# Performance work log

Hardware: AMD Instinct MI355X
Metric: run time of the kernel (lower is better)

## Reference

```python
import jax, jax.numpy as jnp
import numpy as np

B, OBS, ACT, NT, E, H1, H2, D = 4096, 390, 20, 10, 8, 1024, 512, 256


def setup_inputs() -> dict:
    key = jax.random.key(0)
    ks = jax.random.split(key, 16)
    f32 = jnp.float32

    def w(k, shape, fan_in):
        return jax.random.normal(k, shape, f32) / np.float32(np.sqrt(fan_in))

    return {
        "state_feat": jax.random.normal(ks[0], (B, OBS), f32),
        "act": jax.random.normal(ks[1], (B, ACT), f32),
        "task_id": jax.random.randint(ks[2], (B,), 0, NT, jnp.int32),
        "rep_W1": w(ks[3], (OBS + ACT, H1), OBS + ACT),
        "rep_b1": jnp.zeros((H1,), f32),
        "rep_W2": w(ks[4], (H1, H1), H1),
        "rep_b2": jnp.zeros((H1,), f32),
        "emb": 0.5 * jax.random.normal(ks[5], (NT, D), f32),
        "kW1": w(ks[6], (E, H1, H2), H1),
        "kb1": jnp.zeros((E, H2), f32),
        "kW2": w(ks[7], (E, H2, D), H2),
        "kb2": jnp.zeros((E, D), f32),
        "vW1": w(ks[8], (E, H1, H2), H1),
        "vb1": jnp.zeros((E, H2), f32),
        "vW2": w(ks[9], (E, H2, D), H2),
        "vb2": jnp.zeros((E, D), f32),
        "tW1": w(ks[10], (D, D), D),
        "tb1": jnp.zeros((D,), f32),
        "tW2": w(ks[11], (D, D), D),
        "tb2": jnp.zeros((D,), f32),
        "tW3": w(ks[12], (D, 1), D),
        "tb3": jnp.zeros((1,), f32),
    }


def reference(state_feat, act, task_id, rep_W1, rep_b1, rep_W2, rep_b2, emb,
              kW1, kb1, kW2, kb2, vW1, vb1, vW2, vb2,
              tW1, tb1, tW2, tb2, tW3, tb3):
    # representation: mlp([obs+act, 1024, 1024]) -> ReLU on first layer only
    x = jnp.concatenate([state_feat, act], axis=-1)              # [B, 410]
    rep = jnp.maximum(x @ rep_W1 + rep_b1, 0.0) @ rep_W2 + rep_b2  # [B, H1]
    query = jnp.tanh(emb[task_id])                               # [B, D]

    # batched per-expert key/value MLPs (grouped GEMM instead of python loop)
    hk = jnp.maximum(jnp.einsum('bi,eio->ebo', rep, kW1) + kb1[:, None, :], 0.0)
    keys = jnp.einsum('ebo,eod->ebd', hk, kW2) + kb2[:, None, :]   # [E, B, D]
    hv = jnp.maximum(jnp.einsum('bi,eio->ebo', rep, vW1) + vb1[:, None, :], 0.0)
    vals = jnp.einsum('ebo,eod->ebd', hv, vW2) + vb2[:, None, :]   # [E, B, D]

    scores = jnp.einsum('bd,ebd->be', query, keys)               # [B, E]
    weight = jax.nn.softmax(scores, axis=1)                      # [B, E]
    tower_in = jnp.einsum('be,ebd->bd', weight, vals)            # [B, D]

    # tower: mlp([256, 256, 256, 1]) -> ReLU, ReLU, Identity
    h = jnp.maximum(tower_in @ tW1 + tb1, 0.0)
    h = jnp.maximum(h @ tW2 + tb2, 0.0)
    q = (h @ tW3 + tb3)[:, 0]                                    # [B]

    expert_loss = -jnp.mean(
        jnp.sum(jnp.clip(jnp.log(weight + 1e-10), -6.0, 0.0), axis=-1) * 0.3)
    return q, expert_loss
```

## Files before the change

### kernel.cpp

```cpp
#include <hip/hip_runtime.h>

constexpr int Bn   = 4096;
constexpr int OBS  = 390;
constexpr int ACTN = 20;
constexpr int IN   = 410;
constexpr int KPAD = 416;
constexpr int E    = 8;
constexpr int H1   = 1024;
constexpr int H2   = 512;
constexpr int D    = 256;

typedef __bf16 bf16x8 __attribute__((ext_vector_type(8)));
typedef float  f32x4  __attribute__((ext_vector_type(4)));

__device__ __forceinline__ unsigned short f2bf(float f) {
    unsigned int u = __float_as_uint(f);
    unsigned int r = u + 0x7fffu + ((u >> 16) & 1u);
    return (unsigned short)(r >> 16);
}
__device__ __forceinline__ void gload16(void* lds_dst, const void* g_src) {
    __builtin_amdgcn_global_load_lds(
        (const __attribute__((address_space(1))) void*)g_src,
        (__attribute__((address_space(3))) void*)lds_dst,
        16, 0, 0);
}

__global__ void prep_kernel(const float* __restrict__ sf, const float* __restrict__ ac,
                            unsigned short* __restrict__ x,
                            const float* __restrict__ emb, const int* __restrict__ task_id,
                            float* __restrict__ query) {
    int idx = blockIdx.x * blockDim.x + threadIdx.x;
    if (idx < Bn * KPAD) {
        int b = idx / KPAD;
        int k = idx - b * KPAD;
        float v = 0.f;
        if (k < OBS) v = sf[b * OBS + k];
        else if (k < IN) v = ac[b * ACTN + (k - OBS)];
        x[idx] = f2bf(v);
    } else {
        int j = idx - Bn * KPAD;
        int b = j >> 8;
        int d = j & 255;
        query[j] = tanhf(emb[task_id[b] * D + d]);
    }
}

struct TDesc {
    const float* W;
    unsigned short* WT;
    int K, N, Kpad;
    long long gsW, gsO;
    int tilesX, tilesY, perG;
    int start;
};
struct TDescArr { TDesc d[8]; };

__global__ __launch_bounds__(256) void mega_transpose(TDescArr da) {
    int bid = blockIdx.x;
    int i = 0;
#pragma unroll
    for (int j = 1; j < 8; ++j) if (bid >= da.d[j].start) i = j;
    TDesc dd = da.d[i];
    int local = bid - dd.start;
    int g   = local / dd.perG;
    int rem = local - g * dd.perG;
    int tyt = rem / dd.tilesX;
    int txt = rem - tyt * dd.tilesX;
    const float* W = dd.W + (long long)g * dd.gsW;
    unsigned short* WT = dd.WT + (long long)g * dd.gsO;

    __shared__ float tile[32][33];
    int tx = threadIdx.x & 31, ty = threadIdx.x >> 5;
    int k0 = tyt * 32, n0 = txt * 32;
#pragma unroll
    for (int r = 0; r < 4; ++r) {
        int k = k0 + ty + r * 8;
        tile[ty + r * 8][tx] = (k < dd.K) ? W[(long long)k * dd.N + n0 + tx] : 0.f;
    }
    __syncthreads();
#pragma unroll
    for (int r = 0; r < 4; ++r) {
        int n = n0 + ty + r * 8;
        WT[(long long)n * dd.Kpad + k0 + tx] = f2bf(tile[tx][ty + r * 8]);
    }
}

__global__ void bias_concat(const float* __restrict__ kb1, const float* __restrict__ vb1,
                            const float* __restrict__ kb2, const float* __restrict__ vb2,
                            float* __restrict__ b1cat, float* __restrict__ b2cat) {
    int i = blockIdx.x * blockDim.x + threadIdx.x;
    if (i < E * H2)            b1cat[i] = kb1[i];
    else if (i < 2 * E * H2)   b1cat[i] = vb1[i - E * H2];
    else {
        int j = i - 2 * E * H2;
        if (j < E * D)         b2cat[j] = kb2[j];
        else                   b2cat[j] = vb2[j - E * D];
    }
}

template <int ACTF, int OUTF, int BK>
__global__ __launch_bounds__(256) void gemm_bf16(
    const unsigned short* __restrict__ A, const unsigned short* __restrict__ BT,
    const float* __restrict__ bias, void* __restrict__ Cout,
    int K, int ldc,
    long long gsA, long long gsBT, long long gsBias, long long gsC)
{
    constexpr int CH   = BK / 8;
    constexpr int RPR  = 256 / CH;
    constexpr int RNDS = 128 / RPR;
    constexpr int TB   = 128 * BK * 2;
    constexpr int RS   = CH * 16;

    const int g = blockIdx.z;
    A    += (long long)g * gsA;
    BT   += (long long)g * gsBT;
    bias += (long long)g * gsBias;
    float*          Cf = (float*)Cout + (long long)g * gsC;
    unsigned short* Cb = (unsigned short*)Cout + (long long)g * gsC;

    __shared__ alignas(16) char smem[2 * TB];
    const int t  = threadIdx.x;
    const int w  = t >> 6, l = t & 63;
    const int lr = l & 15, lk = l >> 4;
    const int gm = blockIdx.y * 128, gn = blockIdx.x * 128;
    const int wm = (w >> 1) * 64,   wn = (w & 1) * 64;

    const int srow = t / CH;
    const int swzS = (CH == 8) ? (srow & 7) : ((srow >> 1) & 3);
    const int sc   = (t % CH) ^ swzS;
    const unsigned short* gA = A  + (long long)(gm + srow) * K + sc * 8;
    const unsigned short* gB = BT + (long long)(gn + srow) * K + sc * 8;

    const int swzL = (CH == 8) ? (lr & 7) : ((lr >> 1) & 3);
    const int aoff = (wm + lr) * RS + ((lk ^ swzL) * 16);
    const int boff = TB + (wn + lr) * RS + ((lk ^ swzL) * 16);

    f32x4 acc[4][4] = {};

    for (int k0 = 0; k0 < K; k0 += BK) {
#pragma unroll
        for (int j = 0; j < RNDS; ++j) {
            gload16(smem + j * 4096 + w * 1024,      gA + k0 + (long long)j * RPR * K);
            gload16(smem + TB + j * 4096 + w * 1024, gB + k0 + (long long)j * RPR * K);
        }
        __syncthreads();

        bf16x8 af[4], bfr[4];
#pragma unroll
        for (int i = 0; i < 4; ++i) {
            af[i]  = *(const bf16x8*)(smem + aoff + i * 16 * RS);
            bfr[i] = *(const bf16x8*)(smem + boff + i * 16 * RS);
        }
#pragma unroll
        for (int mi = 0; mi < 4; ++mi)
#pragma unroll
            for (int ni = 0; ni < 4; ++ni)
                acc[mi][ni] = __builtin_amdgcn_mfma_f32_16x16x32_bf16(
                    af[mi], bfr[ni], acc[mi][ni], 0, 0, 0);

        if constexpr (BK == 64) {
#pragma unroll
            for (int i = 0; i < 4; ++i) {
                af[i]  = *(const bf16x8*)(smem + (aoff ^ 64) + i * 16 * RS);
                bfr[i] = *(const bf16x8*)(smem + (boff ^ 64) + i * 16 * RS);
            }
#pragma unroll
            for (int mi = 0; mi < 4; ++mi)
#pragma unroll
                for (int ni = 0; ni < 4; ++ni)
                    acc[mi][ni] = __builtin_amdgcn_mfma_f32_16x16x32_bf16(
                        af[mi], bfr[ni], acc[mi][ni], 0, 0, 0);
        }
        __syncthreads();
    }

    const int orow0 = gm + wm + lk * 4;
    const int ocol0 = gn + wn + lr;
    float bv[4];
#pragma unroll
    for (int ni = 0; ni < 4; ++ni) bv[ni] = bias[gn + wn + lr + ni * 16];
#pragma unroll
    for (int mi = 0; mi < 4; ++mi)
#pragma unroll
        for (int ni = 0; ni < 4; ++ni)
#pragma unroll
            for (int r = 0; r < 4; ++r) {
                float v = acc[mi][ni][r] + bv[ni];
                if (ACTF == 1) v = fmaxf(v, 0.f);
                long long off = (long long)(orow0 + mi * 16 + r) * ldc + ocol0 + ni * 16;
                if (OUTF == 0) Cf[off] = v;
                else           Cb[off] = f2bf(v);
            }
}

template <int KTOT, int ACTF, int OUTF>
__global__ __launch_bounds__(512, 2) void gemm256(
    const unsigned short* __restrict__ A, const unsigned short* __restrict__ BT,
    const float* __restrict__ bias, void* __restrict__ Cout,
    int ldc, long long gsA, long long gsBT, long long gsBias, long long gsC)
{
    constexpr int NT = KTOT / 64;
    static_assert(NT >= 4 && (NT % 2) == 0, "KTOT must be multiple of 128");

    const int g = blockIdx.z;
    A    += (long long)g * gsA;
    BT   += (long long)g * gsBT;
    bias += (long long)g * gsBias;
    float*          Cf = (float*)Cout + (long long)g * gsC;
    unsigned short* Cb = (unsigned short*)Cout + (long long)g * gsC;

    __shared__ __align__(16) char smem[131072];

    const int tid = threadIdx.x;
    const int l  = tid & 63;
    const int lr = l & 15, lk = l >> 4;
    const int w  = tid >> 6;
    const int wr = w >> 2, wc = w & 3;
    const int gm = blockIdx.y * 256, gn = blockIdx.x * 256;

    const int srow = tid >> 3;
    const int cg   = (tid & 7) ^ (srow & 7);
    const unsigned short* gA = A  + (long long)(gm + srow) * KTOT + cg * 8;
    const unsigned short* gB = BT + (long long)(gn + srow) * KTOT + cg * 8;
    const int wbase = (tid & ~63) * 16;

    const int cs0 = ((0 | lk) ^ (lr & 7)) * 16;
    const int cs1 = ((4 | lk) ^ (lr & 7)) * 16;
    const int aRow = wr * 16384 + lr * 128;
    const int bRow = 32768 + (wc >> 1) * 16384 + ((wc & 1) * 64 + lr) * 128;

    f32x4 acc[8][4] = {};

    auto stA = [&](int c, int s, int kt) {
        const unsigned short* src = gA + (long long)(s * 128) * KTOT + kt * 64;
        char* d = smem + c * 65536 + s * 16384 + wbase;
        gload16(d,        src);
        gload16(d + 8192, src + (long long)64 * KTOT);
    };
    auto stB = [&](int c, int s, int kt) {
        const unsigned short* src = gB + (long long)(s * 128) * KTOT + kt * 64;
        char* d = smem + c * 65536 + 32768 + s * 16384 + wbase;
        gload16(d,        src);
        gload16(d + 8192, src + (long long)64 * KTOT);
    };

    stA(0, 0, 0); stA(0, 1, 0); stB(0, 0, 0); stB(0, 1, 0);
    stA(1, 0, 1); stA(1, 1, 1);
    asm volatile("s_waitcnt vmcnt(4)" ::: "memory");
    __builtin_amdgcn_s_barrier();
    __builtin_amdgcn_sched_barrier(0);

#pragma unroll
    for (int kt = 0; kt < NT; ++kt) {
        const int c = kt & 1;
        const char* bufc = smem + c * 65536;
        bf16x8 a0[4], a1[4], b0[4], b1[4];

#pragma unroll
        for (int m = 0; m < 4; ++m) {
            const char* base = bufc + aRow + m * (16 * 128);
            a0[m] = *(const bf16x8*)(base + cs0);
            a1[m] = *(const bf16x8*)(base + cs1);
        }
#pragma unroll
        for (int n = 0; n < 4; ++n) {
            const char* base = bufc + bRow + n * (16 * 128);
            b0[n] = *(const bf16x8*)(base + cs0);
            b1[n] = *(const bf16x8*)(base + cs1);
        }
        if (kt + 1 < NT) { stB(c ^ 1, 0, kt + 1); stB(c ^ 1, 1, kt + 1); }
        __builtin_amdgcn_s_setprio(1);
#pragma unroll
        for (int m = 0; m < 4; ++m)
#pragma unroll
            for (int n = 0; n < 4; ++n) {
                acc[m][n] = __builtin_amdgcn_mfma_f32_16x16x32_bf16(a0[m], b0[n], acc[m][n], 0, 0, 0);
                acc[m][n] = __builtin_amdgcn_mfma_f32_16x16x32_bf16(a1[m], b1[n], acc[m][n], 0, 0, 0);
            }
        __builtin_amdgcn_s_setprio(0);

#pragma unroll
        for (int m = 0; m < 4; ++m) {
            const char* base = bufc + aRow + (64 + m * 16) * 128;
            a0[m] = *(const bf16x8*)(base + cs0);
            a1[m] = *(const bf16x8*)(base + cs1);
        }
        asm volatile("s_waitcnt lgkmcnt(0)" ::: "memory");
        __builtin_amdgcn_sched_barrier(0);
        if (kt + 2 < NT) {
            __builtin_amdgcn_s_barrier();
            __builtin_amdgcn_sched_barrier(0);
            stA(c, 0, kt + 2); stA(c, 1, kt + 2);
        }
        __builtin_amdgcn_s_setprio(1);
#pragma unroll
        for (int m = 0; m < 4; ++m)
#pragma unroll
            for (int n = 0; n < 4; ++n) {
                acc[4 + m][n] = __builtin_amdgcn_mfma_f32_16x16x32_bf16(a0[m], b0[n], acc[4 + m][n], 0, 0, 0);
                acc[4 + m][n] = __builtin_amdgcn_mfma_f32_16x16x32_bf16(a1[m], b1[n], acc[4 + m][n], 0, 0, 0);
            }
        __builtin_amdgcn_s_setprio(0);

        if (kt + 1 < NT) {
            if (kt + 2 < NT) { asm volatile("s_waitcnt vmcnt(4)" ::: "memory"); }
            else             { asm volatile("s_waitcnt vmcnt(0)" ::: "memory"); }
            __builtin_amdgcn_sched_barrier(0);
            __builtin_amdgcn_s_barrier();
            __builtin_amdgcn_sched_barrier(0);
        }
    }

    const int orow0 = gm + wr * 128 + lk * 4;
    const int ocol0 = gn + wc * 64 + lr;
    float bv[4];
#pragma unroll
    for (int ni = 0; ni < 4; ++ni) bv[ni] = bias[gn + wc * 64 + lr + ni * 16];
#pragma unroll
    for (int mi = 0; mi < 8; ++mi)
#pragma unroll
        for (int ni = 0; ni < 4; ++ni)
#pragma unroll
            for (int r = 0; r < 4; ++r) {
                float v = acc[mi][ni][r] + bv[ni];
                if (ACTF == 1) v = fmaxf(v, 0.f);
                long long off = (long long)(orow0 + mi * 16 + r) * ldc + ocol0 + ni * 16;
                if (OUTF == 0) Cf[off] = v;
                else           Cb[off] = f2bf(v);
            }
}

__global__ __launch_bounds__(256) void attn_kernel(
    const float* __restrict__ query, const unsigned short* __restrict__ keys,
    const unsigned short* __restrict__ vals, unsigned short* __restrict__ tower_in,
    float* __restrict__ loss_partial)
{
    int wv   = threadIdx.x >> 6;
    int lane = threadIdx.x & 63;
    int b    = blockIdx.x * 4 + wv;
    int d0   = lane * 4;

    const float4 q4 = *(const float4*)&query[(long long)b * D + d0];

    float s[E];
#pragma unroll
    for (int e = 0; e < E; ++e) {
        uint2 kk = *(const uint2*)&keys[((long long)e * Bn + b) * D + d0];
        float k0 = __uint_as_float(kk.x << 16);
        float k1 = __uint_as_float(kk.x & 0xffff0000u);
        float k2 = __uint_as_float(kk.y << 16);
        float k3 = __uint_as_float(kk.y & 0xffff0000u);
        float p = q4.x * k0 + q4.y * k1 + q4.z * k2 + q4.w * k3;
#pragma unroll
        for (int off = 32; off > 0; off >>= 1) p += __shfl_xor(p, off, 64);
        s[e] = p;
    }

    float m = s[0];
#pragma unroll
    for (int e = 1; e < E; ++e) m = fmaxf(m, s[e]);
    float wgt[E];
    float sum = 0.f;
#pragma unroll
    for (int e = 0; e < E; ++e) { wgt[e] = expf(s[e] - m); sum += wgt[e]; }
    float inv = 1.f / sum;

    float4 acc = make_float4(0.f, 0.f, 0.f, 0.f);
    float lb = 0.f;
#pragma unroll
    for (int e = 0; e < E; ++e) {
        float we = wgt[e] * inv;
        uint2 vv = *(const uint2*)&vals[((long long)e * Bn + b) * D + d0];
        acc.x += we * __uint_as_float(vv.x << 16);
        acc.y += we * __uint_as_float(vv.x & 0xffff0000u);
        acc.z += we * __uint_as_float(vv.y << 16);
        acc.w += we * __uint_as_float(vv.y & 0xffff0000u);
        lb += fminf(fmaxf(logf(we + 1e-10f), -6.f), 0.f);
    }
    ushort4 o;
    o.x = f2bf(acc.x); o.y = f2bf(acc.y); o.z = f2bf(acc.z); o.w = f2bf(acc.w);
    *(ushort4*)&tower_in[(long long)b * D + d0] = o;

    __shared__ float sm[4];
    if (lane == 0) sm[wv] = lb;
    __syncthreads();
    if (threadIdx.x == 0)
        loss_partial[blockIdx.x] = sm[0] + sm[1] + sm[2] + sm[3];
}

__global__ __launch_bounds__(256) void qdot_loss_kernel(
    const float* __restrict__ t2, const float* __restrict__ tW3,
    const float* __restrict__ tb3, float* __restrict__ out,
    const float* __restrict__ lossp)
{
    if (blockIdx.x == Bn / 4) {
        float s = 0.f;
        for (int i = threadIdx.x; i < Bn / 4; i += 256) s += lossp[i];
#pragma unroll
        for (int off = 32; off > 0; off >>= 1) s += __shfl_xor(s, off, 64);
        __shared__ float sm[4];
        if ((threadIdx.x & 63) == 0) sm[threadIdx.x >> 6] = s;
        __syncthreads();
        if (threadIdx.x == 0) out[Bn] = (-0.3f / Bn) * (sm[0] + sm[1] + sm[2] + sm[3]);
        return;
    }
    int wv   = threadIdx.x >> 6;
    int lane = threadIdx.x & 63;
    int b    = blockIdx.x * 4 + wv;
    int d0   = lane * 4;
    float4 h4 = *(const float4*)&t2[(long long)b * D + d0];
    float4 w4 = *(const float4*)&tW3[d0];
    float p = h4.x * w4.x + h4.y * w4.y + h4.z * w4.z + h4.w * w4.w;
#pragma unroll
    for (int off = 32; off > 0; off >>= 1) p += __shfl_xor(p, off, 64);
    if (lane == 0) out[b] = p + tb3[0];
}

extern "C" void kernel_launch(void* const* d_in, const int* in_sizes, int n_in,
                              void* d_out, int out_size, void* d_ws, size_t ws_size,
                              hipStream_t stream) {
    const float* state_feat = (const float*)d_in[0];
    const float* act        = (const float*)d_in[1];
    const int*   task_id    = (const int*)d_in[2];
    const float* rep_W1 = (const float*)d_in[3];
    const float* rep_b1 = (const float*)d_in[4];
    const float* rep_W2 = (const float*)d_in[5];
    const float* rep_b2 = (const float*)d_in[6];
    const float* emb    = (const float*)d_in[7];
    const float* kW1 = (const float*)d_in[8];
    const float* kb1 = (const float*)d_in[9];
    const float* kW2 = (const float*)d_in[10];
    const float* kb2 = (const float*)d_in[11];
    const float* vW1 = (const float*)d_in[12];
    const float* vb1 = (const float*)d_in[13];
    const float* vW2 = (const float*)d_in[14];
    const float* vb2 = (const float*)d_in[15];
    const float* tW1 = (const float*)d_in[16];
    const float* tb1 = (const float*)d_in[17];
    const float* tW2 = (const float*)d_in[18];
    const float* tb2 = (const float*)d_in[19];
    const float* tW3 = (const float*)d_in[20];
    const float* tb3 = (const float*)d_in[21];
    float* out = (float*)d_out;

    char* p = (char*)d_ws;
    auto alloc = [&](size_t bytes) {
        char* r = p;
        p += (bytes + 255) & ~(size_t)255;
        return r;
    };
    bool fused = ws_size >= (size_t)150 * 1024 * 1024;

    unsigned short* x      = (unsigned short*)alloc((size_t)Bn * KPAD * 2);
    unsigned short* repW1T = (unsigned short*)alloc((size_t)H1 * KPAD * 2);
    unsigned short* repW2T = (unsigned short*)alloc((size_t)H1 * H1 * 2);
    unsigned short* w1T    = (unsigned short*)alloc((size_t)2 * E * H2 * H1 * 2);
    unsigned short* w2T    = (unsigned short*)alloc((size_t)2 * E * D * H2 * 2);
    unsigned short* tW1T   = (unsigned short*)alloc((size_t)D * D * 2);
    unsigned short* tW2T   = (unsigned short*)alloc((size_t)D * D * 2);
    float*          b1cat  = (float*)alloc((size_t)2 * E * H2 * 4);
    float*          b2cat  = (float*)alloc((size_t)2 * E * D * 4);
    char*           h1zone = alloc((size_t)Bn * H1 * 2);
    unsigned short* rep    = (unsigned short*)alloc((size_t)Bn * H1 * 2);
    unsigned short* hkv    = (unsigned short*)alloc((size_t)(fused ? 2 * E : E) * Bn * H2 * 2);
    unsigned short* kv     = (unsigned short*)alloc((size_t)2 * E * Bn * D * 2);
    float*          query  = (float*)alloc((size_t)Bn * D * 4);
    float*          lossp  = (float*)alloc((size_t)(Bn / 4) * 4);

    unsigned short* h1       = (unsigned short*)h1zone;
    unsigned short* tower_in = (unsigned short*)h1zone;
    unsigned short* t1       = (unsigned short*)(h1zone + (size_t)Bn * D * 2);
    float*          t2       = (float*)(h1zone + (size_t)2 * Bn * D * 2);

    TDescArr da;
    int startAcc = 0;
    auto setd = [&](int i, const float* W, unsigned short* WT, int K, int N, int Kpad,
                    long long gsW, long long gsO, int groups) {
        TDesc& dd = da.d[i];
        dd.W = W; dd.WT = WT; dd.K = K; dd.N = N; dd.Kpad = Kpad;
        dd.gsW = gsW; dd.gsO = gsO;
        dd.tilesX = N / 32; dd.tilesY = Kpad / 32;
        dd.perG = dd.tilesX * dd.tilesY;
        dd.start = startAcc;
        startAcc += dd.perG * groups;
    };
    setd(0, rep_W1, repW1T, IN, H1, KPAD, 0, 0, 1);
    setd(1, rep_W2, repW2T, H1, H1, H1, 0, 0, 1);
    setd(2, kW1, w1T,                       H1, H2, H1, (long long)H1 * H2, (long long)H2 * H1, E);
    setd(3, vW1, w1T + (size_t)E * H2 * H1, H1, H2, H1, (long long)H1 * H2, (long long)H2 * H1, E);
    setd(4, kW2, w2T,                       H2, D, H2, (long long)H2 * D, (long long)D * H2, E);
    setd(5, vW2, w2T + (size_t)E * D * H2,  H2, D, H2, (long long)H2 * D, (long long)D * H2, E);
    setd(6, tW1, tW1T, D, D, D, 0, 0, 1);
    setd(7, tW2, tW2T, D, D, D, 0, 0, 1);
    mega_transpose<<<startAcc, 256, 0, stream>>>(da);

    bias_concat<<<(2 * E * H2 + 2 * E * D) / 256, 256, 0, stream>>>(
        kb1, vb1, kb2, vb2, b1cat, b2cat);
    prep_kernel<<<(Bn * KPAD + Bn * D) / 256, 256, 0, stream>>>(
        state_feat, act, x, emb, task_id, query);

    gemm_bf16<1, 1, 32><<<dim3(H1 / 128, Bn / 128, 1), 256, 0, stream>>>(
        x, repW1T, rep_b1, h1, KPAD, H1, 0, 0, 0, 0);
    gemm_bf16<0, 1, 64><<<dim3(H1 / 128, Bn / 128, 1), 256, 0, stream>>>(
        h1, repW2T, rep_b2, rep, H1, H1, 0, 0, 0, 0);

    if (fused) {
        gemm256<H1, 1, 1><<<dim3(H2 / 256, Bn / 256, 2 * E), 512, 0, stream>>>(
            rep, w1T, b1cat, hkv, H2,
            0, (long long)H2 * H1, H2, (long long)Bn * H2);
        gemm256<H2, 0, 1><<<dim3(D / 256, Bn / 256, 2 * E), 512, 0, stream>>>(
            hkv, w2T, b2cat, kv, D,
            (long long)Bn * H2, (long long)D * H2, D, (long long)Bn * D);
    } else {
        for (int half = 0; half < 2; ++half) {
            gemm256<H1, 1, 1><<<dim3(H2 / 256, Bn / 256, E), 512, 0, stream>>>(
                rep, w1T + (size_t)half * E * H2 * H1, b1cat + half * E * H2, hkv, H2,
                0, (long long)H2 * H1, H2, (long long)Bn * H2);
            gemm256<H2, 0, 1><<<dim3(D / 256, Bn / 256, E), 512, 0, stream>>>(
                hkv, w2T + (size_t)half * E * D * H2, b2cat + half * E * D,
                kv + (size_t)half * E * Bn * D, D,
                (long long)Bn * H2, (long long)D * H2, D, (long long)Bn * D);
        }
    }

    attn_kernel<<<Bn / 4, 256, 0, stream>>>(
        query, kv, kv + (size_t)E * Bn * D, tower_in, lossp);

    gemm_bf16<1, 1, 64><<<dim3(D / 128, Bn / 128, 1), 256, 0, stream>>>(
        tower_in, tW1T, tb1, t1, D, D, 0, 0, 0, 0);
    gemm_bf16<1, 0, 64><<<dim3(D / 128, Bn / 128, 1), 256, 0, stream>>>(
        t1, tW2T, tb2, t2, D, D, 0, 0, 0, 0);

    qdot_loss_kernel<<<Bn / 4 + 1, 256, 0, stream>>>(t2, tW3, tb3, out, lossp);
}
```

Baseline: 174.3 us.

## Restructure gemm256 main loop into quarter-tile MFMA phases with deeper prefetch

The 256x256 grouped GEMM main loop is split into four MFMA phases, each working on half of the B fragments with a smaller register footprint. Barriers between phases interleave LDS reads and global-to-LDS loads for both A and B two k-steps ahead, with prefetch now 8 loads deep. The second expert GEMM (K=512) moves from the 256-tile kernel to the 128-tile gemm_bf16 kernel, which launches more blocks. The extra barriers may cost synchronisation overhead, and the loop is only partly unrolled.

After: 188.0 us. +7.9%, slower.

```diff
diff --git a/kernel.cpp b/kernel.cpp
--- a/kernel.cpp
+++ b/kernel.cpp
@@ -200,7 +200,7 @@
     int ldc, long long gsA, long long gsBT, long long gsBias, long long gsC)
 {
     constexpr int NT = KTOT / 64;
-    static_assert(NT >= 4 && (NT % 2) == 0, "KTOT must be multiple of 128");
+    static_assert(NT >= 2, "KTOT must be >= 128");
 
     const int g = blockIdx.z;
     A    += (long long)g * gsA;
@@ -230,6 +230,7 @@
     const int bRow = 32768 + (wc >> 1) * 16384 + ((wc & 1) * 64 + lr) * 128;
 
     f32x4 acc[8][4] = {};
+    bf16x8 a[4][2], b[4][2];
 
     auto stA = [&](int c, int s, int kt) {
         const unsigned short* src = gA + (long long)(s * 128) * KTOT + kt * 64;
@@ -244,67 +245,100 @@
         gload16(d + 8192, src + (long long)64 * KTOT);
     };
 
-    stA(0, 0, 0); stA(0, 1, 0); stB(0, 0, 0); stB(0, 1, 0);
-    stA(1, 0, 1); stA(1, 1, 1);
-    asm volatile("s_waitcnt vmcnt(4)" ::: "memory");
+    stB(0, 0, 0); stB(0, 1, 0); stA(0, 0, 0); stA(0, 1, 0);
+    stB(1, 0, 1); stB(1, 1, 1); stA(1, 0, 1); stA(1, 1, 1);
+    asm volatile("s_waitcnt vmcnt(8)" ::: "memory");
     __builtin_amdgcn_s_barrier();
     __builtin_amdgcn_sched_barrier(0);
 
-#pragma unroll
+#pragma unroll 2
     for (int kt = 0; kt < NT; ++kt) {
         const int c = kt & 1;
         const char* bufc = smem + c * 65536;
-        bf16x8 a0[4], a1[4], b0[4], b1[4];
+        const bool st = (kt + 2 < NT);
 
 #pragma unroll
         for (int m = 0; m < 4; ++m) {
-            const char* base = bufc + aRow + m * (16 * 128);
-            a0[m] = *(const bf16x8*)(base + cs0);
-            a1[m] = *(const bf16x8*)(base + cs1);
-        }
-#pragma unroll
-        for (int n = 0; n < 4; ++n) {
-            const char* base = bufc + bRow + n * (16 * 128);
-            b0[n] = *(const bf16x8*)(base + cs0);
-            b1[n] = *(const bf16x8*)(base + cs1);
-        }
-        if (kt + 1 < NT) { stB(c ^ 1, 0, kt + 1); stB(c ^ 1, 1, kt + 1); }
+            const char* base = bufc + aRow + m * 2048;
+            a[m][0] = *(const bf16x8*)(base + cs0);
+            a[m][1] = *(const bf16x8*)(base + cs1);
+        }
+#pragma unroll
+        for (int n = 0; n < 2; ++n) {
+            const char* base = bufc + bRow + n * 2048;
+            b[n][0] = *(const bf16x8*)(base + cs0);
+            b[n][1] = *(const bf16x8*)(base + cs1);
+        }
+        __builtin_amdgcn_s_barrier();
         __builtin_amdgcn_s_setprio(1);
 #pragma unroll
-        for (int m = 0; m < 4; ++m)
-#pragma unroll
-            for (int n = 0; n < 4; ++n) {
-                acc[m][n] = __builtin_amdgcn_mfma_f32_16x16x32_bf16(a0[m], b0[n], acc[m][n], 0, 0, 0);
-                acc[m][n] = __builtin_amdgcn_mfma_f32_16x16x32_bf16(a1[m], b1[n], acc[m][n], 0, 0, 0);
-            }
+        for (int ks = 0; ks < 2; ++ks)
+#pragma unroll
+            for (int m = 0; m < 4; ++m)
+#pragma unroll
+                for (int n = 0; n < 2; ++n)
+                    acc[m][n] = __builtin_amdgcn_mfma_f32_16x16x32_bf16(
+                        a[m][ks], b[n][ks], acc[m][n], 0, 0, 0);
         __builtin_amdgcn_s_setprio(0);
+        __builtin_amdgcn_s_barrier();
+
+#pragma unroll
+        for (int n = 2; n < 4; ++n) {
+            const char* base = bufc + bRow + n * 2048;
+            b[n][0] = *(const bf16x8*)(base + cs0);
+            b[n][1] = *(const bf16x8*)(base + cs1);
+        }
+        __builtin_amdgcn_s_barrier();
+        __builtin_amdgcn_s_setprio(1);
+#pragma unroll
+        for (int ks = 0; ks < 2; ++ks)
+#pragma unroll
+            for (int m = 0; m < 4; ++m)
+#pragma unroll
+                for (int n = 2; n < 4; ++n)
+                    acc[m][n] = __builtin_amdgcn_mfma_f32_16x16x32_bf16(
+                        a[m][ks], b[n][ks], acc[m][n], 0, 0, 0);
+        __builtin_amdgcn_s_setprio(0);
+        asm volatile("s_waitcnt lgkmcnt(0)" ::: "memory");
+        __builtin_amdgcn_sched_barrier(0);
+        __builtin_amdgcn_s_barrier();
 
 #pragma unroll
         for (int m = 0; m < 4; ++m) {
             const char* base = bufc + aRow + (64 + m * 16) * 128;
-            a0[m] = *(const bf16x8*)(base + cs0);
-            a1[m] = *(const bf16x8*)(base + cs1);
-        }
+            a[m][0] = *(const bf16x8*)(base + cs0);
+            a[m][1] = *(const bf16x8*)(base + cs1);
+        }
+        if (st) { stB(c, 0, kt + 2); stB(c, 1, kt + 2); }
+        __builtin_amdgcn_s_barrier();
+        __builtin_amdgcn_s_setprio(1);
+#pragma unroll
+        for (int ks = 0; ks < 2; ++ks)
+#pragma unroll
+            for (int m = 0; m < 4; ++m)
+#pragma unroll
+                for (int n = 0; n < 2; ++n)
+                    acc[4 + m][n] = __builtin_amdgcn_mfma_f32_16x16x32_bf16(
+                        a[m][ks], b[n][ks], acc[4 + m][n], 0, 0, 0);
+        __builtin_amdgcn_s_setprio(0);
         asm volatile("s_waitcnt lgkmcnt(0)" ::: "memory");
         __builtin_amdgcn_sched_barrier(0);
-        if (kt + 2 < NT) {
-            __builtin_amdgcn_s_barrier();
-            __builtin_amdgcn_sched_barrier(0);
-            stA(c, 0, kt + 2); stA(c, 1, kt + 2);
-        }
+        __builtin_amdgcn_s_barrier();
+
+        if (st) { stA(c, 0, kt + 2); stA(c, 1, kt + 2); }
         __builtin_amdgcn_s_setprio(1);
 #pragma unroll
-        for (int m = 0; m < 4; ++m)
-#pragma unroll
-            for (int n = 0; n < 4; ++n) {
-                acc[4 + m][n] = __builtin_amdgcn_mfma_f32_16x16x32_bf16(a0[m], b0[n], acc[4 + m][n], 0, 0, 0);
-                acc[4 + m][n] = __builtin_amdgcn_mfma_f32_16x16x32_bf16(a1[m], b1[n], acc[4 + m][n], 0, 0, 0);
-            }
+        for (int ks = 0; ks < 2; ++ks)
+#pragma unroll
+            for (int m = 0; m < 4; ++m)
+#pragma unroll
+                for (int n = 2; n < 4; ++n)
+                    acc[4 + m][n] = __builtin_amdgcn_mfma_f32_16x16x32_bf16(
+                        a[m][ks], b[n][ks], acc[4 + m][n], 0, 0, 0);
         __builtin_amdgcn_s_setprio(0);
-
         if (kt + 1 < NT) {
-            if (kt + 2 < NT) { asm volatile("s_waitcnt vmcnt(4)" ::: "memory"); }
-            else             { asm volatile("s_waitcnt vmcnt(0)" ::: "memory"); }
+            if (st) { asm volatile("s_waitcnt vmcnt(8)" ::: "memory"); }
+            else    { asm volatile("s_waitcnt vmcnt(0)" ::: "memory"); }
             __builtin_amdgcn_sched_barrier(0);
             __builtin_amdgcn_s_barrier();
             __builtin_amdgcn_sched_barrier(0);
@@ -508,17 +542,17 @@
         gemm256<H1, 1, 1><<<dim3(H2 / 256, Bn / 256, 2 * E), 512, 0, stream>>>(
             rep, w1T, b1cat, hkv, H2,
             0, (long long)H2 * H1, H2, (long long)Bn * H2);
-        gemm256<H2, 0, 1><<<dim3(D / 256, Bn / 256, 2 * E), 512, 0, stream>>>(
-            hkv, w2T, b2cat, kv, D,
+        gemm_bf16<0, 1, 64><<<dim3(D / 128, Bn / 128, 2 * E), 256, 0, stream>>>(
+            hkv, w2T, b2cat, kv, H2, D,
             (long long)Bn * H2, (long long)D * H2, D, (long long)Bn * D);
     } else {
         for (int half = 0; half < 2; ++half) {
             gemm256<H1, 1, 1><<<dim3(H2 / 256, Bn / 256, E), 512, 0, stream>>>(
                 rep, w1T + (size_t)half * E * H2 * H1, b1cat + half * E * H2, hkv, H2,
                 0, (long long)H2 * H1, H2, (long long)Bn * H2);
-            gemm256<H2, 0, 1><<<dim3(D / 256, Bn / 256, E), 512, 0, stream>>>(
+            gemm_bf16<0, 1, 64><<<dim3(D / 128, Bn / 128, E), 256, 0, stream>>>(
                 hkv, w2T + (size_t)half * E * D * H2, b2cat + half * E * D,
-                kv + (size_t)half * E * Bn * D, D,
+                kv + (size_t)half * E * Bn * D, H2, D,
                 (long long)Bn * H2, (long long)D * H2, D, (long long)Bn * D);
         }
     }
```

## Fold key second layer into per-task query projection, skip key GEMM

Applied to the files above, without the earlier changes.

Scores are rewritten as hk·(kW2·tanh(emb[t])) + kb2·tanh(emb[t]). A small kernel precomputes the projected query for each expert and task, so the key second-layer GEMM and its weight transpose are removed. The attention kernel now reads the 512-wide hidden keys directly, and the value second layer runs through the 128-tile GEMM. This trades one grouped GEMM for heavier reads of hk in attention and a slightly different rounding path (keys are no longer rounded to bf16).

Result: slower. 188.4 us (+8.1%).

```diff
diff --git a/kernel.cpp b/kernel.cpp
--- a/kernel.cpp
+++ b/kernel.cpp
@@ -6,6 +6,7 @@
 constexpr int IN   = 410;
 constexpr int KPAD = 416;
 constexpr int E    = 8;
+constexpr int NT   = 10;
 constexpr int H1   = 1024;
 constexpr int H2   = 512;
 constexpr int D    = 256;
@@ -17,6 +18,9 @@
     unsigned int u = __float_as_uint(f);
     unsigned int r = u + 0x7fffu + ((u >> 16) & 1u);
     return (unsigned short)(r >> 16);
+}
+__device__ __forceinline__ float bf2f(unsigned short h) {
+    return __uint_as_float(((unsigned int)h) << 16);
 }
 __device__ __forceinline__ void gload16(void* lds_dst, const void* g_src) {
     __builtin_amdgcn_global_load_lds(
@@ -26,22 +30,48 @@
 }
 
 __global__ void prep_kernel(const float* __restrict__ sf, const float* __restrict__ ac,
-                            unsigned short* __restrict__ x,
-                            const float* __restrict__ emb, const int* __restrict__ task_id,
-                            float* __restrict__ query) {
+                            unsigned short* __restrict__ x) {
     int idx = blockIdx.x * blockDim.x + threadIdx.x;
-    if (idx < Bn * KPAD) {
-        int b = idx / KPAD;
-        int k = idx - b * KPAD;
-        float v = 0.f;
-        if (k < OBS) v = sf[b * OBS + k];
-        else if (k < IN) v = ac[b * ACTN + (k - OBS)];
-        x[idx] = f2bf(v);
+    if (idx >= Bn * KPAD) return;
+    int b = idx / KPAD;
+    int k = idx - b * KPAD;
+    float v = 0.f;
+    if (k < OBS) v = sf[b * OBS + k];
+    else if (k < IN) v = ac[b * ACTN + (k - OBS)];
+    x[idx] = f2bf(v);
+}
+
+__global__ __launch_bounds__(256) void qproj_kernel(
+    const float* __restrict__ kW2, const float* __restrict__ kb2,
+    const float* __restrict__ emb, float* __restrict__ qp, float* __restrict__ qb)
+{
+    __shared__ float tq[NT][D];
+    for (int i = threadIdx.x; i < NT * D; i += 256)
+        tq[i / D][i - (i / D) * D] = tanhf(emb[i]);
+    __syncthreads();
+
+    if (blockIdx.x < 16) {
+        int e = blockIdx.x >> 1;
+        int h = (blockIdx.x & 1) * 256 + threadIdx.x;
+        const float4* row = (const float4*)(kW2 + ((long long)e * H2 + h) * D);
+        float acc[NT] = {};
+        for (int d4 = 0; d4 < D / 4; ++d4) {
+            float4 wv = row[d4];
+#pragma unroll
+            for (int t = 0; t < NT; ++t)
+                acc[t] += wv.x * tq[t][d4 * 4] + wv.y * tq[t][d4 * 4 + 1]
+                        + wv.z * tq[t][d4 * 4 + 2] + wv.w * tq[t][d4 * 4 + 3];
+        }
+#pragma unroll
+        for (int t = 0; t < NT; ++t)
+            qp[((long long)e * NT + t) * H2 + h] = acc[t];
     } else {
-        int j = idx - Bn * KPAD;
-        int b = j >> 8;
-        int d = j & 255;
-        query[j] = tanhf(emb[task_id[b] * D + d]);
+        if (threadIdx.x < E * NT) {
+            int e = threadIdx.x / NT, t = threadIdx.x - e * NT;
+            float s = 0.f;
+            for (int d = 0; d < D; ++d) s += kb2[e * D + d] * tq[t][d];
+            qb[e * NT + t] = s;
+        }
     }
 }
 
@@ -86,16 +116,10 @@
 }
 
 __global__ void bias_concat(const float* __restrict__ kb1, const float* __restrict__ vb1,
-                            const float* __restrict__ kb2, const float* __restrict__ vb2,
-                            float* __restrict__ b1cat, float* __restrict__ b2cat) {
+                            float* __restrict__ b1cat) {
     int i = blockIdx.x * blockDim.x + threadIdx.x;
-    if (i < E * H2)            b1cat[i] = kb1[i];
-    else if (i < 2 * E * H2)   b1cat[i] = vb1[i - E * H2];
-    else {
-        int j = i - 2 * E * H2;
-        if (j < E * D)         b2cat[j] = kb2[j];
-        else                   b2cat[j] = vb2[j - E * D];
-    }
+    if (i < E * H2)          b1cat[i] = kb1[i];
+    else if (i < 2 * E * H2) b1cat[i] = vb1[i - E * H2];
 }
 
 template <int ACTF, int OUTF, int BK>
@@ -199,8 +223,8 @@
     const float* __restrict__ bias, void* __restrict__ Cout,
     int ldc, long long gsA, long long gsBT, long long gsBias, long long gsC)
 {
-    constexpr int NT = KTOT / 64;
-    static_assert(NT >= 4 && (NT % 2) == 0, "KTOT must be multiple of 128");
+    constexpr int NT_ = KTOT / 64;
+    static_assert(NT_ >= 4 && (NT_ % 2) == 0, "KTOT must be multiple of 128");
 
     const int g = blockIdx.z;
     A    += (long long)g * gsA;
@@ -251,7 +275,7 @@
     __builtin_amdgcn_sched_barrier(0);
 
 #pragma unroll
-    for (int kt = 0; kt < NT; ++kt) {
+    for (int kt = 0; kt < NT_; ++kt) {
         const int c = kt & 1;
         const char* bufc = smem + c * 65536;
         bf16x8 a0[4], a1[4], b0[4], b1[4];
@@ -268,7 +292,7 @@
             b0[n] = *(const bf16x8*)(base + cs0);
             b1[n] = *(const bf16x8*)(base + cs1);
         }
-        if (kt + 1 < NT) { stB(c ^ 1, 0, kt + 1); stB(c ^ 1, 1, kt + 1); }
+        if (kt + 1 < NT_) { stB(c ^ 1, 0, kt + 1); stB(c ^ 1, 1, kt + 1); }
         __builtin_amdgcn_s_setprio(1);
 #pragma unroll
         for (int m = 0; m < 4; ++m)
@@ -287,7 +311,7 @@
         }
         asm volatile("s_waitcnt lgkmcnt(0)" ::: "memory");
         __builtin_amdgcn_sched_barrier(0);
-        if (kt + 2 < NT) {
+        if (kt + 2 < NT_) {
             __builtin_amdgcn_s_barrier();
             __builtin_amdgcn_sched_barrier(0);
             stA(c, 0, kt + 2); stA(c, 1, kt + 2);
@@ -302,9 +326,9 @@
             }
         __builtin_amdgcn_s_setprio(0);
 
-        if (kt + 1 < NT) {
-            if (kt + 2 < NT) { asm volatile("s_waitcnt vmcnt(4)" ::: "memory"); }
-            else             { asm volatile("s_waitcnt vmcnt(0)" ::: "memory"); }
+        if (kt + 1 < NT_) {
+            if (kt + 2 < NT_) { asm volatile("s_waitcnt vmcnt(4)" ::: "memory"); }
+            else              { asm volatile("s_waitcnt vmcnt(0)" ::: "memory"); }
             __builtin_amdgcn_sched_barrier(0);
             __builtin_amdgcn_s_barrier();
             __builtin_amdgcn_sched_barrier(0);
@@ -330,30 +354,31 @@
             }
 }
 
-__global__ __launch_bounds__(256) void attn_kernel(
-    const float* __restrict__ query, const unsigned short* __restrict__ keys,
-    const unsigned short* __restrict__ vals, unsigned short* __restrict__ tower_in,
+__global__ __launch_bounds__(256) void attn_score_kernel(
+    const unsigned short* __restrict__ hk, const unsigned short* __restrict__ vals,
+    const float* __restrict__ qp, const float* __restrict__ qb,
+    const int* __restrict__ task_id, unsigned short* __restrict__ tower_in,
     float* __restrict__ loss_partial)
 {
     int wv   = threadIdx.x >> 6;
     int lane = threadIdx.x & 63;
     int b    = blockIdx.x * 4 + wv;
-    int d0   = lane * 4;
-
-    const float4 q4 = *(const float4*)&query[(long long)b * D + d0];
+    int t    = task_id[b];
 
     float s[E];
 #pragma unroll
     for (int e = 0; e < E; ++e) {
-        uint2 kk = *(const uint2*)&keys[((long long)e * Bn + b) * D + d0];
-        float k0 = __uint_as_float(kk.x << 16);
-        float k1 = __uint_as_float(kk.x & 0xffff0000u);
-        float k2 = __uint_as_float(kk.y << 16);
-        float k3 = __uint_as_float(kk.y & 0xffff0000u);
-        float p = q4.x * k0 + q4.y * k1 + q4.z * k2 + q4.w * k3;
+        const ushort4 h4a = *(const ushort4*)&hk[((long long)e * Bn + b) * H2 + lane * 8];
+        const ushort4 h4b = *(const ushort4*)&hk[((long long)e * Bn + b) * H2 + lane * 8 + 4];
+        const float4 q4a = *(const float4*)&qp[((long long)e * NT + t) * H2 + lane * 8];
+        const float4 q4b = *(const float4*)&qp[((long long)e * NT + t) * H2 + lane * 8 + 4];
+        float p = bf2f(h4a.x) * q4a.x + bf2f(h4a.y) * q4a.y
+                + bf2f(h4a.z) * q4a.z + bf2f(h4a.w) * q4a.w
+                + bf2f(h4b.x) * q4b.x + bf2f(h4b.y) * q4b.y
+                + bf2f(h4b.z) * q4b.z + bf2f(h4b.w) * q4b.w;
 #pragma unroll
         for (int off = 32; off > 0; off >>= 1) p += __shfl_xor(p, off, 64);
-        s[e] = p;
+        s[e] = p + qb[e * NT + t];
     }
 
     float m = s[0];
@@ -365,6 +390,7 @@
     for (int e = 0; e < E; ++e) { wgt[e] = expf(s[e] - m); sum += wgt[e]; }
     float inv = 1.f / sum;
 
+    int d0 = lane * 4;
     float4 acc = make_float4(0.f, 0.f, 0.f, 0.f);
     float lb = 0.f;
 #pragma unroll
@@ -449,28 +475,28 @@
         p += (bytes + 255) & ~(size_t)255;
         return r;
     };
-    bool fused = ws_size >= (size_t)150 * 1024 * 1024;
-
     unsigned short* x      = (unsigned short*)alloc((size_t)Bn * KPAD * 2);
     unsigned short* repW1T = (unsigned short*)alloc((size_t)H1 * KPAD * 2);
     unsigned short* repW2T = (unsigned short*)alloc((size_t)H1 * H1 * 2);
     unsigned short* w1T    = (unsigned short*)alloc((size_t)2 * E * H2 * H1 * 2);
-    unsigned short* w2T    = (unsigned short*)alloc((size_t)2 * E * D * H2 * 2);
+    unsigned short* w2T    = (unsigned short*)alloc((size_t)E * D * H2 * 2);
     unsigned short* tW1T   = (unsigned short*)alloc((size_t)D * D * 2);
     unsigned short* tW2T   = (unsigned short*)alloc((size_t)D * D * 2);
     float*          b1cat  = (float*)alloc((size_t)2 * E * H2 * 4);
-    float*          b2cat  = (float*)alloc((size_t)2 * E * D * 4);
+    float*          qp     = (float*)alloc((size_t)E * NT * H2 * 4);
+    float*          qb     = (float*)alloc((size_t)E * NT * 4);
     char*           h1zone = alloc((size_t)Bn * H1 * 2);
     unsigned short* rep    = (unsigned short*)alloc((size_t)Bn * H1 * 2);
-    unsigned short* hkv    = (unsigned short*)alloc((size_t)(fused ? 2 * E : E) * Bn * H2 * 2);
-    unsigned short* kv     = (unsigned short*)alloc((size_t)2 * E * Bn * D * 2);
-    float*          query  = (float*)alloc((size_t)Bn * D * 4);
+    unsigned short* hkv    = (unsigned short*)alloc((size_t)2 * E * Bn * H2 * 2);
+    unsigned short* vals   = (unsigned short*)alloc((size_t)E * Bn * D * 2);
     float*          lossp  = (float*)alloc((size_t)(Bn / 4) * 4);
 
     unsigned short* h1       = (unsigned short*)h1zone;
     unsigned short* tower_in = (unsigned short*)h1zone;
     unsigned short* t1       = (unsigned short*)(h1zone + (size_t)Bn * D * 2);
     float*          t2       = (float*)(h1zone + (size_t)2 * Bn * D * 2);
+    unsigned short* hk = hkv;
+    unsigned short* hv = hkv + (size_t)E * Bn * H2;
 
     TDescArr da;
     int startAcc = 0;
@@ -488,43 +514,31 @@
     setd(1, rep_W2, repW2T, H1, H1, H1, 0, 0, 1);
     setd(2, kW1, w1T,                       H1, H2, H1, (long long)H1 * H2, (long long)H2 * H1, E);
     setd(3, vW1, w1T + (size_t)E * H2 * H1, H1, H2, H1, (long long)H1 * H2, (long long)H2 * H1, E);
-    setd(4, kW2, w2T,                       H2, D, H2, (long long)H2 * D, (long long)D * H2, E);
-    setd(5, vW2, w2T + (size_t)E * D * H2,  H2, D, H2, (long long)H2 * D, (long long)D * H2, E);
-    setd(6, tW1, tW1T, D, D, D, 0, 0, 1);
-    setd(7, tW2, tW2T, D, D, D, 0, 0, 1);
+    setd(4, vW2, w2T,                       H2, D, H2, (long long)H2 * D, (long long)D * H2, E);
+    setd(5, tW1, tW1T, D, D, D, 0, 0, 1);
+    setd(6, tW2, tW2T, D, D, D, 0, 0, 1);
+    da.d[7] = da.d[6];
+    da.d[7].start = 0x7fffffff;
     mega_transpose<<<startAcc, 256, 0, stream>>>(da);
 
-    bias_concat<<<(2 * E * H2 + 2 * E * D) / 256, 256, 0, stream>>>(
-        kb1, vb1, kb2, vb2, b1cat, b2cat);
-    prep_kernel<<<(Bn * KPAD + Bn * D) / 256, 256, 0, stream>>>(
-        state_feat, act, x, emb, task_id, query);
+    bias_concat<<<(2 * E * H2) / 256, 256, 0, stream>>>(kb1, vb1, b1cat);
+    prep_kernel<<<(Bn * KPAD + 255) / 256, 256, 0, stream>>>(state_feat, act, x);
+    qproj_kernel<<<17, 256, 0, stream>>>(kW2, kb2, emb, qp, qb);
 
     gemm_bf16<1, 1, 32><<<dim3(H1 / 128, Bn / 128, 1), 256, 0, stream>>>(
         x, repW1T, rep_b1, h1, KPAD, H1, 0, 0, 0, 0);
     gemm_bf16<0, 1, 64><<<dim3(H1 / 128, Bn / 128, 1), 256, 0, stream>>>(
         h1, repW2T, rep_b2, rep, H1, H1, 0, 0, 0, 0);
 
-    if (fused) {
-        gemm256<H1, 1, 1><<<dim3(H2 / 256, Bn / 256, 2 * E), 512, 0, stream>>>(
-            rep, w1T, b1cat, hkv, H2,
-            0, (long long)H2 * H1, H2, (long long)Bn * H2);
-        gemm256<H2, 0, 1><<<dim3(D / 256, Bn / 256, 2 * E), 512, 0, stream>>>(
-            hkv, w2T, b2cat, kv, D,
-            (long long)Bn * H2, (long long)D * H2, D, (long long)Bn * D);
-    } else {
-        for (int half = 0; half < 2; ++half) {
-            gemm256<H1, 1, 1><<<dim3(H2 / 256, Bn / 256, E), 512, 0, stream>>>(
-                rep, w1T + (size_t)half * E * H2 * H1, b1cat + half * E * H2, hkv, H2,
-                0, (long long)H2 * H1, H2, (long long)Bn * H2);
-            gemm256<H2, 0, 1><<<dim3(D / 256, Bn / 256, E), 512, 0, stream>>>(
-                hkv, w2T + (size_t)half * E * D * H2, b2cat + half * E * D,
-                kv + (size_t)half * E * Bn * D, D,
-                (long long)Bn * H2, (long long)D * H2, D, (long long)Bn * D);
-        }
-    }
-
-    attn_kernel<<<Bn / 4, 256, 0, stream>>>(
-        query, kv, kv + (size_t)E * Bn * D, tower_in, lossp);
+    gemm256<H1, 1, 1><<<dim3(H2 / 256, Bn / 256, 2 * E), 512, 0, stream>>>(
+        rep, w1T, b1cat, hkv, H2,
+        0, (long long)H2 * H1, H2, (long long)Bn * H2);
+    gemm_bf16<0, 1, 64><<<dim3(D / 128, Bn / 128, E), 256, 0, stream>>>(
+        hv, w2T, vb2, vals, H2, D,
+        (long long)Bn * H2, (long long)D * H2, D, (long long)Bn * D);
+
+    attn_score_kernel<<<Bn / 4, 256, 0, stream>>>(
+        hk, vals, qp, qb, task_id, tower_in, lossp);
 
     gemm_bf16<1, 1, 64><<<dim3(D / 128, Bn / 128, 1), 256, 0, stream>>>(
         tower_in, tW1T, tb1, t1, D, D, 0, 0, 0, 0);
```
